# Kernel tuning notes

Hardware: AMD Instinct MI355X
Metric: run time of the kernel (lower is better)

## Reference

```python
import jax, jax.numpy as jnp
import numpy as np

EPS = 1e-8  # torch.nn.CosineSimilarity default eps

def setup_inputs() -> dict:
    key = jax.random.key(0)
    k1, k2 = jax.random.split(key)
    B, R, T, D = 256, 36, 64, 1024
    img_feats = jax.random.normal(k1, (B, R, D), dtype=jnp.float32)
    cap_feats = jax.random.normal(k2, (B, T, D), dtype=jnp.float32)
    cap_mask = jnp.ones((B, T), dtype=jnp.float32)  # unused by the original forward
    return {"img_feats": img_feats, "cap_feats": cap_feats, "cap_mask": cap_mask}

def reference(img_feats, cap_feats, cap_mask):
    # img_feats: (B, R, D); cap_feats: (B, T, D)
    # cosine similarity between every region r and every caption word t:
    # scores[b, r, t] = (img[b,r] . cap[b,t]) / max(||img[b,r]|| * ||cap[b,t]||, eps)
    dots = jnp.einsum('brd,btd->brt', img_feats, cap_feats)
    img_norm = jnp.linalg.norm(img_feats, axis=-1)  # (B, R)
    cap_norm = jnp.linalg.norm(cap_feats, axis=-1)  # (B, T)
    denom = jnp.maximum(img_norm[:, :, None] * cap_norm[:, None, :], EPS)
    scores = dots / denom  # (B, R, T)
    # softmax over regions (dim=1 in the original)
    attn = jax.nn.softmax(scores, axis=1)  # (B, R, T)
    # weighted sum over regions -> per-word image representation (B, T, D)
    img_cap_reps = jnp.einsum('brt,brd->btd', attn, img_feats)
    return img_cap_reps
```

## Files before the change

### kernel.cpp

```cpp
#include <hip/hip_runtime.h>
#include <hip/hip_bf16.h>

#define DDIM 1024
#define RREG 36
#define TTOK 64
#define KPAD 48
#define CHUNK 256
#define LSTR 264

typedef __attribute__((ext_vector_type(4))) float f32x4;
typedef __attribute__((ext_vector_type(8))) short bf16x8;

__device__ __forceinline__ float sq4(float4 v) {
  return v.x * v.x + v.y * v.y + v.z * v.z + v.w * v.w;
}

__device__ __forceinline__ ushort4 cvt4(float4 v) {
  union { ushort4 u; __hip_bfloat162 h[2]; } r;
  r.h[0] = __float22bfloat162_rn(make_float2(v.x, v.y));
  r.h[1] = __float22bfloat162_rn(make_float2(v.z, v.w));
  return r.u;
}

__device__ __forceinline__ bf16x8 pack8(const float* v) {
  union { bf16x8 x; __hip_bfloat162 h[4]; } u;
#pragma unroll
  for (int i = 0; i < 4; ++i)
    u.h[i] = __float22bfloat162_rn(make_float2(v[2 * i], v[2 * i + 1]));
  return u.x;
}

__device__ __forceinline__ unsigned short f2bf(float x) {
  unsigned int u = __float_as_uint(x);
  u += 0x7fffu + ((u >> 16) & 1u);
  return (unsigned short)(u >> 16);
}

__global__ __launch_bounds__(256) void scan_attn(
    const float* __restrict__ img, const float* __restrict__ cap,
    unsigned short* __restrict__ attnw) {
  __shared__ unsigned short scap[16 * LSTR];
  __shared__ unsigned short simg[48 * LSTR];
  __shared__ float sdots[16][52];
  __shared__ float sni[KPAD];
  __shared__ float snc[16];

  const int tid  = threadIdx.x;
  const int lane = tid & 63;
  const int wave = tid >> 6;
  const int fm   = lane & 15;
  const int kq   = lane >> 4;
  const int b    = blockIdx.x >> 2;
  const int t0   = (blockIdx.x & 3) << 4;

  const float* capb = cap + (size_t)b * TTOK * DDIM;
  const float* imgb = img + (size_t)b * RREG * DDIM;

  {
    ushort4 zz; zz.x = 0; zz.y = 0; zz.z = 0; zz.w = 0;
    for (int i = tid; i < 792; i += 256)
      *(ushort4*)(simg + 36 * LSTR + i * 4) = zz;
  }

  const int u = tid >> 2;
  const int q = tid & 3;
  const bool active = (u < 52);
  const bool is_cap = (u < 16);
  const float* srcrow = is_cap ? (capb + (size_t)(t0 + u) * DDIM)
                               : (imgb + (size_t)(active ? (u - 16) : 0) * DDIM);
  unsigned short* dstrow = is_cap ? (scap + u * LSTR) : (simg + (u - 16) * LSTR);

  float nrm = 0.f;
  f32x4 acc = {0.f, 0.f, 0.f, 0.f};

  for (int c = 0; c < 4; ++c) {
    if (c) __syncthreads();
    if (active) {
#pragma unroll
      for (int s = 0; s < 16; ++s) {
        const int col = s * 16 + q * 4;
        float4 v = *(const float4*)(srcrow + c * CHUNK + col);
        nrm += sq4(v);
        *(ushort4*)(dstrow + col) = cvt4(v);
      }
    }
    __syncthreads();
    if (wave < 3) {
      const unsigned short* arow = scap + fm * LSTR + kq * 8;
      const unsigned short* brow = simg + (wave * 16 + fm) * LSTR + kq * 8;
#pragma unroll
      for (int ks = 0; ks < 8; ++ks) {
        bf16x8 av = *(const bf16x8*)(arow + ks * 32);
        bf16x8 bv = *(const bf16x8*)(brow + ks * 32);
        acc = __builtin_amdgcn_mfma_f32_16x16x32_bf16(av, bv, acc, 0, 0, 0);
      }
    }
  }

  nrm += __shfl_xor(nrm, 1);
  nrm += __shfl_xor(nrm, 2);
  if (active && q == 0) {
    if (is_cap) snc[u] = sqrtf(nrm);
    else        sni[u - 16] = sqrtf(nrm);
  }
  if (wave < 3) {
#pragma unroll
    for (int i = 0; i < 4; ++i)
      sdots[kq * 4 + i][wave * 16 + fm] = acc[i];
  }
  __syncthreads();

  if (tid < 16) {
    const float cnv = snc[tid];
    float sc[RREG];
    float mx = -1e30f;
#pragma unroll
    for (int rr = 0; rr < RREG; ++rr) {
      float dnm = fmaxf(sni[rr] * cnv, 1e-8f);
      float v = sdots[tid][rr] / dnm;
      sc[rr] = v;
      mx = fmaxf(mx, v);
    }
    float sum = 0.f;
#pragma unroll
    for (int rr = 0; rr < RREG; ++rr) {
      float ev = __expf(sc[rr] - mx);
      sc[rr] = ev;
      sum += ev;
    }
    const float rinv = 1.f / sum;
    unsigned short* arow = attnw + ((size_t)b * TTOK + t0 + tid) * KPAD;
#pragma unroll
    for (int r0 = 0; r0 < RREG; r0 += 4) {
      ushort4 p;
      p.x = f2bf(sc[r0 + 0] * rinv);
      p.y = f2bf(sc[r0 + 1] * rinv);
      p.z = f2bf(sc[r0 + 2] * rinv);
      p.w = f2bf(sc[r0 + 3] * rinv);
      *(ushort4*)(arow + r0) = p;
    }
    ushort4 zz; zz.x = 0; zz.y = 0; zz.z = 0; zz.w = 0;
    *(ushort4*)(arow + 36) = zz;
    *(ushort4*)(arow + 40) = zz;
    *(ushort4*)(arow + 44) = zz;
  }
}

__global__ __launch_bounds__(256) void scan_out(
    const float* __restrict__ img, const unsigned short* __restrict__ attnw,
    float* __restrict__ out) {
  const int tid  = threadIdx.x;
  const int lane = tid & 63;
  const int wave = tid >> 6;
  const int fm   = lane & 15;
  const int kq   = lane >> 4;
  const int b    = blockIdx.x >> 2;
  const int d0   = (blockIdx.x & 3) << 8;

  const float* imgb = img + (size_t)b * RREG * DDIM;
  const unsigned short* attb = attnw + (size_t)b * TTOK * KPAD;
  float* outb = out + (size_t)b * TTOK * DDIM;

  const unsigned short* ap = attb + (wave * 16 + fm) * KPAD;
  bf16x8 zf = {0, 0, 0, 0, 0, 0, 0, 0};
  bf16x8 af0 = *(const bf16x8*)(ap + kq * 8);
  bf16x8 af1 = zf;
  if (kq < 2) af1 = *(const bf16x8*)(ap + 32 + kq * 8);

  for (int s = 0; s < 16; ++s) {
    const int d = d0 + s * 16 + fm;
    float v[8];
#pragma unroll
    for (int j = 0; j < 8; ++j) v[j] = imgb[(kq * 8 + j) * DDIM + d];
    bf16x8 bf0 = pack8(v);
    bf16x8 bf1 = zf;
    if (kq == 0) {
      float w[8];
#pragma unroll
      for (int j = 0; j < 4; ++j) w[j] = imgb[(32 + j) * DDIM + d];
#pragma unroll
      for (int j = 4; j < 8; ++j) w[j] = 0.f;
      bf1 = pack8(w);
    }
    f32x4 o = {0.f, 0.f, 0.f, 0.f};
    o = __builtin_amdgcn_mfma_f32_16x16x32_bf16(af0, bf0, o, 0, 0, 0);
    o = __builtin_amdgcn_mfma_f32_16x16x32_bf16(af1, bf1, o, 0, 0, 0);
    float* op = outb + (wave * 16 + kq * 4) * DDIM + d;
#pragma unroll
    for (int i = 0; i < 4; ++i) op[i * DDIM] = o[i];
  }
}

extern "C" void kernel_launch(void* const* d_in, const int* in_sizes, int n_in,
                              void* d_out, int out_size, void* d_ws, size_t ws_size,
                              hipStream_t stream) {
  const float* img = (const float*)d_in[0];
  const float* cap = (const float*)d_in[1];
  float* out = (float*)d_out;
  unsigned short* attnw = (unsigned short*)d_ws;

  scan_attn<<<dim3(1024), dim3(256), 0, stream>>>(img, cap, attnw);
  scan_out<<<dim3(1024), dim3(256), 0, stream>>>(img, attnw, out);
}
```

Measured before the change: 170.1 us.

## Split score GEMM across waves by K-slice with per-wave LDS and no block barriers

The attention-score kernel now gives each of the four waves its own quarter of the feature dimension. Each wave stages its cap and img slices into a private LDS region and runs three MFMA tiles covering all 36 regions, so the per-chunk block-wide barriers are replaced by a wave-local waitcnt. Partial dot products and norms are then reduced across waves through shared memory before the softmax. Before, one wave sat idle during the MFMA step and loads were serialized behind barriers. The change adds register pressure (9 img float4 per chunk plus three accumulators) and a cross-wave reduction step.

```diff
diff --git a/kernel.cpp b/kernel.cpp
--- a/kernel.cpp
+++ b/kernel.cpp
@@ -5,8 +5,6 @@
 #define RREG 36
 #define TTOK 64
 #define KPAD 48
-#define CHUNK 256
-#define LSTR 264
 
 typedef __attribute__((ext_vector_type(4))) float f32x4;
 typedef __attribute__((ext_vector_type(8))) short bf16x8;
@@ -36,14 +34,10 @@
   return (unsigned short)(u >> 16);
 }
 
-__global__ __launch_bounds__(256) void scan_attn(
+__global__ __launch_bounds__(256, 4) void scan_attn(
     const float* __restrict__ img, const float* __restrict__ cap,
     unsigned short* __restrict__ attnw) {
-  __shared__ unsigned short scap[16 * LSTR];
-  __shared__ unsigned short simg[48 * LSTR];
-  __shared__ float sdots[16][52];
-  __shared__ float sni[KPAD];
-  __shared__ float snc[16];
+  __shared__ __align__(16) unsigned char smem[36864];
 
   const int tid  = threadIdx.x;
   const int lane = tid & 63;
@@ -53,96 +47,146 @@
   const int b    = blockIdx.x >> 2;
   const int t0   = (blockIdx.x & 3) << 4;
 
-  const float* capb = cap + (size_t)b * TTOK * DDIM;
+  const float* capb = cap + (size_t)b * TTOK * DDIM + (size_t)t0 * DDIM;
   const float* imgb = img + (size_t)b * RREG * DDIM;
 
+  unsigned short* Aw = (unsigned short*)smem + wave * 4608;
+  unsigned short* Bw = Aw + 1152;
+
   {
-    ushort4 zz; zz.x = 0; zz.y = 0; zz.z = 0; zz.w = 0;
-    for (int i = tid; i < 792; i += 256)
-      *(ushort4*)(simg + 36 * LSTR + i * 4) = zz;
-  }
-
-  const int u = tid >> 2;
-  const int q = tid & 3;
-  const bool active = (u < 52);
-  const bool is_cap = (u < 16);
-  const float* srcrow = is_cap ? (capb + (size_t)(t0 + u) * DDIM)
-                               : (imgb + (size_t)(active ? (u - 16) : 0) * DDIM);
-  unsigned short* dstrow = is_cap ? (scap + u * LSTR) : (simg + (u - 16) * LSTR);
-
-  float nrm = 0.f;
-  f32x4 acc = {0.f, 0.f, 0.f, 0.f};
-
+    unsigned int* bz = (unsigned int*)(Bw + 36 * 72);
+    for (int z = lane; z < 432; z += 64) bz[z] = 0u;
+  }
+
+  const int ar = lane >> 2;
+  const int aq = lane & 3;
+
+  float an = 0.f;
+  float bn[9];
+#pragma unroll
+  for (int i = 0; i < 9; ++i) bn[i] = 0.f;
+
+  f32x4 acc0 = {0.f, 0.f, 0.f, 0.f};
+  f32x4 acc1 = {0.f, 0.f, 0.f, 0.f};
+  f32x4 acc2 = {0.f, 0.f, 0.f, 0.f};
+
+  const int kbase = wave * 256;
+#pragma unroll 1
   for (int c = 0; c < 4; ++c) {
-    if (c) __syncthreads();
-    if (active) {
-#pragma unroll
-      for (int s = 0; s < 16; ++s) {
-        const int col = s * 16 + q * 4;
-        float4 v = *(const float4*)(srcrow + c * CHUNK + col);
-        nrm += sq4(v);
-        *(ushort4*)(dstrow + col) = cvt4(v);
+    const int koff = kbase + c * 64;
+    float4 avd[4], bvd[9];
+#pragma unroll
+    for (int i = 0; i < 4; ++i)
+      avd[i] = *(const float4*)(capb + ar * DDIM + koff + i * 16 + aq * 4);
+#pragma unroll
+    for (int i = 0; i < 9; ++i)
+      bvd[i] = *(const float4*)(imgb + (4 * i + kq) * DDIM + koff + fm * 4);
+#pragma unroll
+    for (int i = 0; i < 4; ++i) {
+      an += sq4(avd[i]);
+      *(ushort4*)(Aw + ar * 72 + i * 16 + aq * 4) = cvt4(avd[i]);
+    }
+#pragma unroll
+    for (int i = 0; i < 9; ++i) {
+      bn[i] += sq4(bvd[i]);
+      *(ushort4*)(Bw + (4 * i + kq) * 72 + fm * 4) = cvt4(bvd[i]);
+    }
+    asm volatile("s_waitcnt lgkmcnt(0)" ::: "memory");
+#pragma unroll
+    for (int ks = 0; ks < 2; ++ks) {
+      bf16x8 af = *(const bf16x8*)(Aw + fm * 72 + ks * 32 + kq * 8);
+      bf16x8 b0 = *(const bf16x8*)(Bw + fm * 72 + ks * 32 + kq * 8);
+      bf16x8 b1 = *(const bf16x8*)(Bw + (16 + fm) * 72 + ks * 32 + kq * 8);
+      bf16x8 b2 = *(const bf16x8*)(Bw + (32 + fm) * 72 + ks * 32 + kq * 8);
+      acc0 = __builtin_amdgcn_mfma_f32_16x16x32_bf16(af, b0, acc0, 0, 0, 0);
+      acc1 = __builtin_amdgcn_mfma_f32_16x16x32_bf16(af, b1, acc1, 0, 0, 0);
+      acc2 = __builtin_amdgcn_mfma_f32_16x16x32_bf16(af, b2, acc2, 0, 0, 0);
+    }
+  }
+
+  an += __shfl_xor(an, 1);
+  an += __shfl_xor(an, 2);
+#pragma unroll
+  for (int i = 0; i < 9; ++i) {
+    bn[i] += __shfl_xor(bn[i], 1);
+    bn[i] += __shfl_xor(bn[i], 2);
+    bn[i] += __shfl_xor(bn[i], 4);
+    bn[i] += __shfl_xor(bn[i], 8);
+  }
+
+  __syncthreads();
+  float* sdots = (float*)smem;
+  float* scapn = (float*)(smem + 13312);
+  float* simgn = (float*)(smem + 13568);
+
+  if (aq == 0) scapn[wave * 16 + ar] = an;
+  if (fm == 0) {
+#pragma unroll
+    for (int i = 0; i < 9; ++i) simgn[wave * 48 + 4 * i + kq] = bn[i];
+  }
+  {
+    float* dp = sdots + wave * 832;
+#pragma unroll
+    for (int i = 0; i < 4; ++i) {
+      dp[(kq * 4 + i) * 52 + fm]      = acc0[i];
+      dp[(kq * 4 + i) * 52 + 16 + fm] = acc1[i];
+      dp[(kq * 4 + i) * 52 + 32 + fm] = acc2[i];
+    }
+  }
+  __syncthreads();
+
+  if (wave == 0) {
+    if (lane < 36) {
+      float s = simgn[lane] + simgn[48 + lane] + simgn[96 + lane] + simgn[144 + lane];
+      simgn[lane] = sqrtf(s);
+    } else if (lane >= 48) {
+      int t = lane - 48;
+      float s = scapn[t] + scapn[16 + t] + scapn[32 + t] + scapn[48 + t];
+      scapn[t] = sqrtf(s);
+    }
+    const int t  = lane & 15;
+    const int rb = lane >> 4;
+    float nc = scapn[t];
+#pragma unroll
+    for (int e = 0; e < 9; ++e) {
+      int r = rb + 4 * e;
+      float d = sdots[t * 52 + r] + sdots[832 + t * 52 + r] +
+                sdots[1664 + t * 52 + r] + sdots[2496 + t * 52 + r];
+      float dn = fmaxf(simgn[r] * nc, 1e-8f);
+      sdots[t * 52 + r] = __fdividef(d, dn);
+    }
+    if (lane < 16) {
+      float sc[RREG];
+      float mx = -1e30f;
+#pragma unroll
+      for (int r = 0; r < RREG; ++r) {
+        float v = sdots[lane * 52 + r];
+        sc[r] = v;
+        mx = fmaxf(mx, v);
       }
-    }
-    __syncthreads();
-    if (wave < 3) {
-      const unsigned short* arow = scap + fm * LSTR + kq * 8;
-      const unsigned short* brow = simg + (wave * 16 + fm) * LSTR + kq * 8;
-#pragma unroll
-      for (int ks = 0; ks < 8; ++ks) {
-        bf16x8 av = *(const bf16x8*)(arow + ks * 32);
-        bf16x8 bv = *(const bf16x8*)(brow + ks * 32);
-        acc = __builtin_amdgcn_mfma_f32_16x16x32_bf16(av, bv, acc, 0, 0, 0);
+      float sum = 0.f;
+#pragma unroll
+      for (int r = 0; r < RREG; ++r) {
+        float ev = __expf(sc[r] - mx);
+        sc[r] = ev;
+        sum += ev;
       }
-    }
-  }
-
-  nrm += __shfl_xor(nrm, 1);
-  nrm += __shfl_xor(nrm, 2);
-  if (active && q == 0) {
-    if (is_cap) snc[u] = sqrtf(nrm);
-    else        sni[u - 16] = sqrtf(nrm);
-  }
-  if (wave < 3) {
-#pragma unroll
-    for (int i = 0; i < 4; ++i)
-      sdots[kq * 4 + i][wave * 16 + fm] = acc[i];
-  }
-  __syncthreads();
-
-  if (tid < 16) {
-    const float cnv = snc[tid];
-    float sc[RREG];
-    float mx = -1e30f;
-#pragma unroll
-    for (int rr = 0; rr < RREG; ++rr) {
-      float dnm = fmaxf(sni[rr] * cnv, 1e-8f);
-      float v = sdots[tid][rr] / dnm;
-      sc[rr] = v;
-      mx = fmaxf(mx, v);
-    }
-    float sum = 0.f;
-#pragma unroll
-    for (int rr = 0; rr < RREG; ++rr) {
-      float ev = __expf(sc[rr] - mx);
-      sc[rr] = ev;
-      sum += ev;
-    }
-    const float rinv = 1.f / sum;
-    unsigned short* arow = attnw + ((size_t)b * TTOK + t0 + tid) * KPAD;
-#pragma unroll
-    for (int r0 = 0; r0 < RREG; r0 += 4) {
-      ushort4 p;
-      p.x = f2bf(sc[r0 + 0] * rinv);
-      p.y = f2bf(sc[r0 + 1] * rinv);
-      p.z = f2bf(sc[r0 + 2] * rinv);
-      p.w = f2bf(sc[r0 + 3] * rinv);
-      *(ushort4*)(arow + r0) = p;
-    }
-    ushort4 zz; zz.x = 0; zz.y = 0; zz.z = 0; zz.w = 0;
-    *(ushort4*)(arow + 36) = zz;
-    *(ushort4*)(arow + 40) = zz;
-    *(ushort4*)(arow + 44) = zz;
+      const float rinv = 1.f / sum;
+      unsigned short* arow = attnw + ((size_t)b * TTOK + t0 + lane) * KPAD;
+#pragma unroll
+      for (int r0 = 0; r0 < RREG; r0 += 4) {
+        ushort4 p;
+        p.x = f2bf(sc[r0 + 0] * rinv);
+        p.y = f2bf(sc[r0 + 1] * rinv);
+        p.z = f2bf(sc[r0 + 2] * rinv);
+        p.w = f2bf(sc[r0 + 3] * rinv);
+        *(ushort4*)(arow + r0) = p;
+      }
+      ushort4 zz; zz.x = 0; zz.y = 0; zz.z = 0; zz.w = 0;
+      *(ushort4*)(arow + 36) = zz;
+      *(ushort4*)(arow + 40) = zz;
+      *(ushort4*)(arow + 44) = zz;
+    }
   }
 }
 
```

Result: no change. 172.9 us (+1.6%).
